# Optimization experiments

Hardware: AMD Instinct MI355X
Metric: run time of the kernel (lower is better)

Reference implementation:

```python
import jax, jax.numpy as jnp
import numpy as np

N_NODES = 50000
N_EDGES = 800000
D = 128


def _gcn_layer(x, src, dst, deg_inv_sqrt, W, b, n_nodes):
    # GCNConv: X' = D^{-1/2} (A + I) D^{-1/2} X W + b   (PyG default, self-loops added)
    h = x @ W  # [N, D]
    norm = deg_inv_sqrt[src] * deg_inv_sqrt[dst]  # [E+N]
    msgs = h[src] * norm[:, None]  # [E+N, D] gather + scale
    out = jax.ops.segment_sum(msgs, dst, num_segments=n_nodes)  # scatter-add
    return out + b


def setup_inputs() -> dict:
    key = jax.random.key(0)
    k1, k2, k3, k4 = jax.random.split(key, 4)
    x = jax.random.normal(k1, (N_NODES, D), dtype=jnp.float32)
    edge_index = jax.random.randint(k2, (2, N_EDGES), 0, N_NODES, dtype=jnp.int64)
    scale = 1.0 / np.sqrt(D)
    W1 = jax.random.normal(k3, (D, D), dtype=jnp.float32) * scale
    b1 = jnp.zeros((D,), dtype=jnp.float32)
    W2 = jax.random.normal(k4, (D, D), dtype=jnp.float32) * scale
    b2 = jnp.zeros((D,), dtype=jnp.float32)
    return {"x": x, "edge_index": edge_index, "W1": W1, "b1": b1, "W2": W2, "b2": b2}


def reference(x, edge_index, W1, b1, W2, b2):
    n_nodes = x.shape[0]
    # add self-loops once (same graph both layers)
    loop = jnp.arange(n_nodes, dtype=edge_index.dtype)
    src = jnp.concatenate([edge_index[0], loop])
    dst = jnp.concatenate([edge_index[1], loop])
    deg = jax.ops.segment_sum(jnp.ones_like(dst, dtype=x.dtype), dst, num_segments=n_nodes)
    deg_inv_sqrt = jnp.where(deg > 0, jax.lax.rsqrt(deg), 0.0)

    h = _gcn_layer(x, src, dst, deg_inv_sqrt, W1, b1, n_nodes)
    h = jax.nn.relu(h)
    h = _gcn_layer(h, src, dst, deg_inv_sqrt, W2, b2, n_nodes)
    h = jax.nn.relu(h)
    return h
```

## Files before the change

### kernel.cpp

```cpp
#include <hip/hip_runtime.h>

#define N_NODES 50000
#define N_EDGES 800000
#define D 128
#define NBKT 391
#define ACB 196
#define ACCHUNK 4096
#define BKTPAD 2432
#define GB 391
#define PB 3125
#define MAXDEG 64

typedef unsigned int uint32;
typedef unsigned short ushort;
typedef __attribute__((ext_vector_type(8))) short s8v;
typedef __attribute__((ext_vector_type(4))) float f4v;

__device__ __forceinline__ ushort f2bf(float f) {
    unsigned u = __float_as_uint(f);
    u += 0x7FFFu + ((u >> 16) & 1u);
    return (ushort)(u >> 16);
}
__device__ __forceinline__ float bf_lo(uint32 u) { return __uint_as_float(u << 16); }
__device__ __forceinline__ float bf_hi(uint32 u) { return __uint_as_float(u & 0xFFFF0000u); }

__global__ __launch_bounds__(256) void prep_kernel(int* __restrict__ bktCnt,
                                                   const float* __restrict__ W1,
                                                   const float* __restrict__ W2,
                                                   ushort* __restrict__ W1t,
                                                   ushort* __restrict__ W2t) {
    int t = threadIdx.x, blk = blockIdx.x;
    if (blk == 32) {
        for (int i = t; i < NBKT; i += 256) bktCnt[i] = 0;
        return;
    }
    const float* W = (blk >= 16) ? W2 : W1;
    ushort* Wt = (blk >= 16) ? W2t : W1t;
    int fid = (blk & 15) * 256 + t;
    int k = fid >> 5;
    int n0 = (fid & 31) * 4;
    float4 w = ((const float4*)W)[fid];
    Wt[(n0 + 0) * D + k] = f2bf(w.x);
    Wt[(n0 + 1) * D + k] = f2bf(w.y);
    Wt[(n0 + 2) * D + k] = f2bf(w.z);
    Wt[(n0 + 3) * D + k] = f2bf(w.w);
}

__global__ __launch_bounds__(256) void phaseAC_kernel(const int* __restrict__ src,
                                                      const int* __restrict__ dst,
                                                      int* __restrict__ bktCnt,
                                                      uint32* __restrict__ edgeTmp) {
    __shared__ int lc[NBKT];
    __shared__ int gb[NBKT];
    int t = threadIdx.x, blk = blockIdx.x;
    for (int i = t; i < NBKT; i += 256) lc[i] = 0;
    __syncthreads();
    uint32 ed[16];
    int e0 = blk * ACCHUNK;
    #pragma unroll
    for (int j = 0; j < 16; j++) {
        int e = e0 + t + j * 256;
        uint32 pk = 0xFFFFFFFFu;
        if (e < N_EDGES) {
            uint32 s = (uint32)src[e], d = (uint32)dst[e];
            pk = (s << 16) | d;
            atomicAdd(&lc[d >> 7], 1);
        }
        ed[j] = pk;
    }
    __syncthreads();
    for (int i = t; i < NBKT; i += 256) {
        int c = lc[i];
        gb[i] = (c > 0) ? atomicAdd(&bktCnt[i], c) : 0;
        lc[i] = 0;
    }
    __syncthreads();
    #pragma unroll
    for (int j = 0; j < 16; j++) {
        uint32 pk = ed[j];
        if (pk != 0xFFFFFFFFu) {
            int bkt = (int)(pk & 0xFFFFu) >> 7;
            int r = atomicAdd(&lc[bkt], 1);
            int idx = gb[bkt] + r;
            if (idx < BKTPAD) edgeTmp[bkt * BKTPAD + idx] = pk;
        }
    }
}

__global__ __launch_bounds__(256) void phaseDG_kernel(const uint32* __restrict__ edgeTmp,
                                                      const int* __restrict__ bktCnt,
                                                      int* __restrict__ deg,
                                                      ushort* __restrict__ e16,
                                                      const float* __restrict__ X,
                                                      const ushort* __restrict__ Wt,
                                                      ushort* __restrict__ Hb) {
    __shared__ int cnt[128];
    __shared__ int cur[128];
    __shared__ float disS[128];
    __shared__ ushort Cs[128 * 136];
    int t = threadIdx.x, b = blockIdx.x;
    int ce = bktCnt[b];
    int cntE = ce < BKTPAD ? ce : BKTPAD;
    int beg = b * BKTPAD, end = beg + cntE;
    if (t < 128) { cnt[t] = 0; cur[t] = 0; }
    __syncthreads();
    for (int p = beg + t; p < end; p += 256)
        atomicAdd(&cnt[edgeTmp[p] & 127], 1);
    __syncthreads();
    int node = b * 128 + t;
    if (t < 128) {
        int c = cnt[t];
        if (node < N_NODES) deg[node] = c;
        disS[t] = rsqrtf((float)c + 1.0f);
    }
    __syncthreads();
    for (int p = beg + t; p < end; p += 256) {
        uint32 u = edgeTmp[p];
        int loc = u & 127;
        int r = atomicAdd(&cur[loc], 1);
        if (r < MAXDEG) e16[((b * 128 + loc) << 6) + r] = (ushort)(u >> 16);
    }
    int wv = t >> 6, lane = t & 63;
    int q = lane >> 4, m = lane & 15;
    int rbase = b * 128 + wv * 32;
    f4v zero = {0.f, 0.f, 0.f, 0.f};
    f4v acc[2][8];
    #pragma unroll
    for (int mt = 0; mt < 2; mt++)
        #pragma unroll
        for (int n = 0; n < 8; n++) acc[mt][n] = zero;
    #pragma unroll
    for (int kt = 0; kt < 4; kt++) {
        int k0 = kt * 32 + q * 8;
        s8v a[2];
        #pragma unroll
        for (int mt = 0; mt < 2; mt++) {
            int row = rbase + mt * 16 + m;
            if (row >= N_NODES) row = N_NODES - 1;
            const float* xp = X + (size_t)row * D + k0;
            float4 u0 = *(const float4*)xp;
            float4 u1 = *(const float4*)(xp + 4);
            s8v av;
            av[0] = (short)f2bf(u0.x); av[1] = (short)f2bf(u0.y);
            av[2] = (short)f2bf(u0.z); av[3] = (short)f2bf(u0.w);
            av[4] = (short)f2bf(u1.x); av[5] = (short)f2bf(u1.y);
            av[6] = (short)f2bf(u1.z); av[7] = (short)f2bf(u1.w);
            a[mt] = av;
        }
        #pragma unroll
        for (int n = 0; n < 8; n++) {
            s8v bb = *(const s8v*)(Wt + (size_t)(n * 16 + m) * D + k0);
            acc[0][n] = __builtin_amdgcn_mfma_f32_16x16x32_bf16(a[0], bb, acc[0][n], 0, 0, 0);
            acc[1][n] = __builtin_amdgcn_mfma_f32_16x16x32_bf16(a[1], bb, acc[1][n], 0, 0, 0);
        }
    }
    __syncthreads();
    #pragma unroll
    for (int mt = 0; mt < 2; mt++)
        #pragma unroll
        for (int n = 0; n < 8; n++)
            #pragma unroll
            for (int r = 0; r < 4; r++) {
                int lr = wv * 32 + mt * 16 + q * 4 + r;
                Cs[lr * 136 + n * 16 + m] = f2bf(acc[mt][n][r] * disS[lr]);
            }
    __syncthreads();
    int gbase = b * 128;
    #pragma unroll
    for (int it = 0; it < 8; it++) {
        int cid = t + it * 256;
        int row = cid >> 4, off = (cid & 15) * 8;
        int grow = gbase + row;
        if (grow < N_NODES) {
            s8v v = *(const s8v*)(Cs + row * 136 + off);
            *(s8v*)(Hb + (size_t)grow * D + off) = v;
        }
    }
}

__global__ __launch_bounds__(256) void gemm_mfma(const ushort* __restrict__ Xb,
                                                 const ushort* __restrict__ Wt,
                                                 const int* __restrict__ deg,
                                                 ushort* __restrict__ Hb) {
    __shared__ ushort Cs[128 * 136];
    int t = threadIdx.x;
    int wv = t >> 6, lane = t & 63;
    int q = lane >> 4, m = lane & 15;
    int rbase = blockIdx.x * 128 + wv * 32;
    f4v zero = {0.f, 0.f, 0.f, 0.f};
    f4v acc[2][8];
    #pragma unroll
    for (int mt = 0; mt < 2; mt++)
        #pragma unroll
        for (int n = 0; n < 8; n++) acc[mt][n] = zero;

    #pragma unroll
    for (int kt = 0; kt < 4; kt++) {
        int k0 = kt * 32 + q * 8;
        s8v a[2];
        #pragma unroll
        for (int mt = 0; mt < 2; mt++) {
            int row = rbase + mt * 16 + m;
            if (row >= N_NODES) row = N_NODES - 1;
            a[mt] = *(const s8v*)(Xb + (size_t)row * D + k0);
        }
        #pragma unroll
        for (int n = 0; n < 8; n++) {
            s8v b = *(const s8v*)(Wt + (size_t)(n * 16 + m) * D + k0);
            acc[0][n] = __builtin_amdgcn_mfma_f32_16x16x32_bf16(a[0], b, acc[0][n], 0, 0, 0);
            acc[1][n] = __builtin_amdgcn_mfma_f32_16x16x32_bf16(a[1], b, acc[1][n], 0, 0, 0);
        }
    }
    float disv[2][4];
    #pragma unroll
    for (int mt = 0; mt < 2; mt++)
        #pragma unroll
        for (int r = 0; r < 4; r++) {
            int row = rbase + mt * 16 + q * 4 + r;
            if (row >= N_NODES) row = N_NODES - 1;
            disv[mt][r] = rsqrtf((float)deg[row] + 1.0f);
        }
    #pragma unroll
    for (int mt = 0; mt < 2; mt++)
        #pragma unroll
        for (int n = 0; n < 8; n++)
            #pragma unroll
            for (int r = 0; r < 4; r++) {
                int row = wv * 32 + mt * 16 + q * 4 + r;
                Cs[row * 136 + n * 16 + m] = f2bf(acc[mt][n][r] * disv[mt][r]);
            }
    __syncthreads();
    int gbase = blockIdx.x * 128;
    #pragma unroll
    for (int it = 0; it < 8; it++) {
        int cid = t + it * 256;
        int row = cid >> 4, off = (cid & 15) * 8;
        int grow = gbase + row;
        if (grow < N_NODES) {
            s8v v = *(const s8v*)(Cs + row * 136 + off);
            *(s8v*)(Hb + (size_t)grow * D + off) = v;
        }
    }
}

__device__ __forceinline__ void acc8(float* a, uint4 v) {
    a[0] += bf_lo(v.x); a[1] += bf_hi(v.x);
    a[2] += bf_lo(v.y); a[3] += bf_hi(v.y);
    a[4] += bf_lo(v.z); a[5] += bf_hi(v.z);
    a[6] += bf_lo(v.w); a[7] += bf_hi(v.w);
}

template<bool BF16OUT>
__global__ __launch_bounds__(256) void aggr_kernel(const uint4* __restrict__ Hb4,
                                                   const int* __restrict__ deg,
                                                   const ushort* __restrict__ e16,
                                                   const float* __restrict__ bias,
                                                   void* __restrict__ Hout) {
    int t = threadIdx.x;
    int li = t & 15;
    int n = blockIdx.x * 16 + (t >> 4);
    int dg = deg[n];
    float dn = rsqrtf((float)dg + 1.0f);
    float a[8];
    {
        uint4 sv = Hb4[(size_t)n * 16 + li];
        a[0] = bf_lo(sv.x); a[1] = bf_hi(sv.x);
        a[2] = bf_lo(sv.y); a[3] = bf_hi(sv.y);
        a[4] = bf_lo(sv.z); a[5] = bf_hi(sv.z);
        a[6] = bf_lo(sv.w); a[7] = bf_hi(sv.w);
    }
    int beg = n << 6;
    int end = beg + (dg < MAXDEG ? dg : MAXDEG);
    int p = beg;
    for (; p + 7 < end; p += 8) {
        int s[8];
        #pragma unroll
        for (int j = 0; j < 8; j++) s[j] = e16[p + j];
        uint4 v[8];
        #pragma unroll
        for (int j = 0; j < 8; j++) v[j] = Hb4[(size_t)s[j] * 16 + li];
        #pragma unroll
        for (int j = 0; j < 8; j++) acc8(a, v[j]);
    }
    for (; p + 3 < end; p += 4) {
        int s0 = e16[p + 0], s1 = e16[p + 1], s2 = e16[p + 2], s3 = e16[p + 3];
        uint4 v0 = Hb4[(size_t)s0 * 16 + li];
        uint4 v1 = Hb4[(size_t)s1 * 16 + li];
        uint4 v2 = Hb4[(size_t)s2 * 16 + li];
        uint4 v3 = Hb4[(size_t)s3 * 16 + li];
        acc8(a, v0); acc8(a, v1); acc8(a, v2); acc8(a, v3);
    }
    for (; p < end; p++) {
        uint4 v0 = Hb4[(size_t)e16[p] * 16 + li];
        acc8(a, v0);
    }
    const float4* b4 = (const float4*)bias;
    float4 bb0 = b4[li * 2], bb1 = b4[li * 2 + 1];
    float r0 = fmaxf(fmaf(dn, a[0], bb0.x), 0.f);
    float r1 = fmaxf(fmaf(dn, a[1], bb0.y), 0.f);
    float r2 = fmaxf(fmaf(dn, a[2], bb0.z), 0.f);
    float r3 = fmaxf(fmaf(dn, a[3], bb0.w), 0.f);
    float r4 = fmaxf(fmaf(dn, a[4], bb1.x), 0.f);
    float r5 = fmaxf(fmaf(dn, a[5], bb1.y), 0.f);
    float r6 = fmaxf(fmaf(dn, a[6], bb1.z), 0.f);
    float r7 = fmaxf(fmaf(dn, a[7], bb1.w), 0.f);
    if (BF16OUT) {
        uint4 o;
        o.x = (uint32)f2bf(r0) | ((uint32)f2bf(r1) << 16);
        o.y = (uint32)f2bf(r2) | ((uint32)f2bf(r3) << 16);
        o.z = (uint32)f2bf(r4) | ((uint32)f2bf(r5) << 16);
        o.w = (uint32)f2bf(r6) | ((uint32)f2bf(r7) << 16);
        ((uint4*)Hout)[(size_t)n * 16 + li] = o;
    } else {
        float4* H4 = (float4*)Hout;
        float4 o0; o0.x = r0; o0.y = r1; o0.z = r2; o0.w = r3;
        float4 o1; o1.x = r4; o1.y = r5; o1.z = r6; o1.w = r7;
        H4[(size_t)n * 32 + li * 2]     = o0;
        H4[(size_t)n * 32 + li * 2 + 1] = o1;
    }
}

extern "C" void kernel_launch(void* const* d_in, const int* in_sizes, int n_in,
                              void* d_out, int out_size, void* d_ws, size_t ws_size,
                              hipStream_t stream) {
    const float* x  = (const float*)d_in[0];
    const int*   ei = (const int*)d_in[1];
    const float* W1 = (const float*)d_in[2];
    const float* b1 = (const float*)d_in[3];
    const float* W2 = (const float*)d_in[4];
    const float* b2 = (const float*)d_in[5];
    float* out = (float*)d_out;

    char* ws = (char*)d_ws;
    size_t off = 0;
    auto alloc = [&](size_t bytes) -> void* {
        void* p = ws + off;
        off += (bytes + 255) & ~(size_t)255;
        return p;
    };
    int*    bktCnt  = (int*)alloc((size_t)NBKT * 4);
    uint32* edgeTmp = (uint32*)alloc((size_t)NBKT * BKTPAD * 4);
    int*    deg     = (int*)alloc((size_t)N_NODES * 4);
    ushort* e16     = (ushort*)alloc((size_t)N_NODES * MAXDEG * 2);
    ushort* Hb      = (ushort*)alloc((size_t)N_NODES * D * 2);
    ushort* HO1     = (ushort*)alloc((size_t)N_NODES * D * 2);
    ushort* W1t     = (ushort*)alloc((size_t)D * D * 2);
    ushort* W2t     = (ushort*)alloc((size_t)D * D * 2);
    ushort* Hb2     = Hb;

    const int* src = ei;
    const int* dst = ei + N_EDGES;

    prep_kernel<<<33, 256, 0, stream>>>(bktCnt, W1, W2, W1t, W2t);
    phaseAC_kernel<<<ACB, 256, 0, stream>>>(src, dst, bktCnt, edgeTmp);
    phaseDG_kernel<<<NBKT, 256, 0, stream>>>(edgeTmp, bktCnt, deg, e16, x, W1t, Hb);
    aggr_kernel<true><<<PB, 256, 0, stream>>>((const uint4*)Hb, deg, e16, b1, HO1);
    gemm_mfma<<<GB, 256, 0, stream>>>(HO1, W2t, deg, Hb2);
    aggr_kernel<false><<<PB, 256, 0, stream>>>((const uint4*)Hb2, deg, e16, b2, out);
}
```

Measured before the change: 200.7 us.

## Partition each node's neighbor list into four source-index ranges for gather locality

The CSR build now counts each node's edges in four chunks by source-node range and places them in range order, with per-chunk counts packed into a uint32 deg4 array. The aggregation kernel walks the neighbor list chunk by chunk, so concurrently running nodes tend to gather from the same quarter of the feature table at the same time, which should improve L2 locality. In exchange the 8-wide unrolled gather loop is dropped for a 4-wide loop per chunk. Packing counts into 8 bits assumes no chunk holds more than 255 edges for a node.

```diff
diff --git a/kernel.cpp b/kernel.cpp
--- a/kernel.cpp
+++ b/kernel.cpp
@@ -10,6 +10,7 @@
 #define GB 391
 #define PB 3125
 #define MAXDEG 64
+#define CHN 12500
 
 typedef unsigned int uint32;
 typedef unsigned short ushort;
@@ -90,35 +91,46 @@
 __global__ __launch_bounds__(256) void phaseDG_kernel(const uint32* __restrict__ edgeTmp,
                                                       const int* __restrict__ bktCnt,
                                                       int* __restrict__ deg,
+                                                      uint32* __restrict__ deg4,
                                                       ushort* __restrict__ e16,
                                                       const float* __restrict__ X,
                                                       const ushort* __restrict__ Wt,
                                                       ushort* __restrict__ Hb) {
-    __shared__ int cnt[128];
-    __shared__ int cur[128];
+    __shared__ int cnt4[128][4];
+    __shared__ int cur4[128][4];
     __shared__ float disS[128];
     __shared__ ushort Cs[128 * 136];
     int t = threadIdx.x, b = blockIdx.x;
     int ce = bktCnt[b];
     int cntE = ce < BKTPAD ? ce : BKTPAD;
     int beg = b * BKTPAD, end = beg + cntE;
-    if (t < 128) { cnt[t] = 0; cur[t] = 0; }
-    __syncthreads();
-    for (int p = beg + t; p < end; p += 256)
-        atomicAdd(&cnt[edgeTmp[p] & 127], 1);
+    if (t < 128) { cnt4[t][0] = 0; cnt4[t][1] = 0; cnt4[t][2] = 0; cnt4[t][3] = 0; }
+    __syncthreads();
+    for (int p = beg + t; p < end; p += 256) {
+        uint32 u = edgeTmp[p];
+        int ch = (int)(u >> 16) / CHN;
+        atomicAdd(&cnt4[u & 127][ch], 1);
+    }
     __syncthreads();
     int node = b * 128 + t;
     if (t < 128) {
-        int c = cnt[t];
-        if (node < N_NODES) deg[node] = c;
-        disS[t] = rsqrtf((float)c + 1.0f);
+        int c0 = cnt4[t][0], c1 = cnt4[t][1], c2 = cnt4[t][2], c3 = cnt4[t][3];
+        int tot = c0 + c1 + c2 + c3;
+        if (node < N_NODES) {
+            deg[node] = tot;
+            deg4[node] = (uint32)c0 | ((uint32)c1 << 8) | ((uint32)c2 << 16)
+                       | ((uint32)c3 << 24);
+        }
+        disS[t] = rsqrtf((float)tot + 1.0f);
+        cur4[t][0] = 0; cur4[t][1] = c0; cur4[t][2] = c0 + c1; cur4[t][3] = c0 + c1 + c2;
     }
     __syncthreads();
     for (int p = beg + t; p < end; p += 256) {
         uint32 u = edgeTmp[p];
         int loc = u & 127;
-        int r = atomicAdd(&cur[loc], 1);
-        if (r < MAXDEG) e16[((b * 128 + loc) << 6) + r] = (ushort)(u >> 16);
+        int s = (int)(u >> 16);
+        int r = atomicAdd(&cur4[loc][s / CHN], 1);
+        if (r < MAXDEG) e16[((b * 128 + loc) << 6) + r] = (ushort)s;
     }
     int wv = t >> 6, lane = t & 63;
     int q = lane >> 4, m = lane & 15;
@@ -252,15 +264,17 @@
 
 template<bool BF16OUT>
 __global__ __launch_bounds__(256) void aggr_kernel(const uint4* __restrict__ Hb4,
-                                                   const int* __restrict__ deg,
+                                                   const uint32* __restrict__ deg4v,
                                                    const ushort* __restrict__ e16,
                                                    const float* __restrict__ bias,
                                                    void* __restrict__ Hout) {
     int t = threadIdx.x;
     int li = t & 15;
     int n = blockIdx.x * 16 + (t >> 4);
-    int dg = deg[n];
-    float dn = rsqrtf((float)dg + 1.0f);
+    uint32 d4 = deg4v[n];
+    int cc0 = d4 & 255, cc1 = (d4 >> 8) & 255, cc2 = (d4 >> 16) & 255, cc3 = d4 >> 24;
+    int tot = cc0 + cc1 + cc2 + cc3;
+    float dn = rsqrtf((float)tot + 1.0f);
     float a[8];
     {
         uint4 sv = Hb4[(size_t)n * 16 + li];
@@ -270,29 +284,25 @@
         a[6] = bf_lo(sv.w); a[7] = bf_hi(sv.w);
     }
     int beg = n << 6;
-    int end = beg + (dg < MAXDEG ? dg : MAXDEG);
+    int cap = beg + MAXDEG;
+    int cc[4] = {cc0, cc1, cc2, cc3};
     int p = beg;
-    for (; p + 7 < end; p += 8) {
-        int s[8];
-        #pragma unroll
-        for (int j = 0; j < 8; j++) s[j] = e16[p + j];
-        uint4 v[8];
-        #pragma unroll
-        for (int j = 0; j < 8; j++) v[j] = Hb4[(size_t)s[j] * 16 + li];
-        #pragma unroll
-        for (int j = 0; j < 8; j++) acc8(a, v[j]);
-    }
-    for (; p + 3 < end; p += 4) {
-        int s0 = e16[p + 0], s1 = e16[p + 1], s2 = e16[p + 2], s3 = e16[p + 3];
-        uint4 v0 = Hb4[(size_t)s0 * 16 + li];
-        uint4 v1 = Hb4[(size_t)s1 * 16 + li];
-        uint4 v2 = Hb4[(size_t)s2 * 16 + li];
-        uint4 v3 = Hb4[(size_t)s3 * 16 + li];
-        acc8(a, v0); acc8(a, v1); acc8(a, v2); acc8(a, v3);
-    }
-    for (; p < end; p++) {
-        uint4 v0 = Hb4[(size_t)e16[p] * 16 + li];
-        acc8(a, v0);
+    #pragma unroll 1
+    for (int ch = 0; ch < 4; ch++) {
+        int e2 = p + cc[ch];
+        if (e2 > cap) e2 = cap;
+        for (; p + 3 < e2; p += 4) {
+            int s0 = e16[p + 0], s1 = e16[p + 1], s2 = e16[p + 2], s3 = e16[p + 3];
+            uint4 v0 = Hb4[(size_t)s0 * 16 + li];
+            uint4 v1 = Hb4[(size_t)s1 * 16 + li];
+            uint4 v2 = Hb4[(size_t)s2 * 16 + li];
+            uint4 v3 = Hb4[(size_t)s3 * 16 + li];
+            acc8(a, v0); acc8(a, v1); acc8(a, v2); acc8(a, v3);
+        }
+        for (; p < e2; p++) {
+            uint4 v0 = Hb4[(size_t)e16[p] * 16 + li];
+            acc8(a, v0);
+        }
     }
     const float4* b4 = (const float4*)bias;
     float4 bb0 = b4[li * 2], bb1 = b4[li * 2 + 1];
@@ -341,6 +351,7 @@
     int*    bktCnt  = (int*)alloc((size_t)NBKT * 4);
     uint32* edgeTmp = (uint32*)alloc((size_t)NBKT * BKTPAD * 4);
     int*    deg     = (int*)alloc((size_t)N_NODES * 4);
+    uint32* deg4    = (uint32*)alloc((size_t)N_NODES * 4);
     ushort* e16     = (ushort*)alloc((size_t)N_NODES * MAXDEG * 2);
     ushort* Hb      = (ushort*)alloc((size_t)N_NODES * D * 2);
     ushort* HO1     = (ushort*)alloc((size_t)N_NODES * D * 2);
@@ -353,8 +364,9 @@
 
     prep_kernel<<<33, 256, 0, stream>>>(bktCnt, W1, W2, W1t, W2t);
     phaseAC_kernel<<<ACB, 256, 0, stream>>>(src, dst, bktCnt, edgeTmp);
-    phaseDG_kernel<<<NBKT, 256, 0, stream>>>(edgeTmp, bktCnt, deg, e16, x, W1t, Hb);
-    aggr_kernel<true><<<PB, 256, 0, stream>>>((const uint4*)Hb, deg, e16, b1, HO1);
+    phaseDG_kernel<<<NBKT, 256, 0, stream>>>(edgeTmp, bktCnt, deg, deg4, e16,
+                                             x, W1t, Hb);
+    aggr_kernel<true><<<PB, 256, 0, stream>>>((const uint4*)Hb, deg4, e16, b1, HO1);
     gemm_mfma<<<GB, 256, 0, stream>>>(HO1, W2t, deg, Hb2);
-    aggr_kernel<false><<<PB, 256, 0, stream>>>((const uint4*)Hb2, deg, e16, b2, out);
-}
+    aggr_kernel<false><<<PB, 256, 0, stream>>>((const uint4*)Hb2, deg4, e16, b2, out);
+}
```

Measured after the change: 201.9 us. About the same (+0.6%).

## Fuse layer-1 aggregation with layer-2 GEMM in one kernel

Applied to the files above, without the earlier changes.

Merges the first aggregation kernel and the second-layer MFMA GEMM into a single kernel. Each 16-node block stages its aggregated bf16 rows in shared memory, multiplies them by W2 with MFMA, scales by the degree normalisation and writes Hb2. This removes one launch and the HBM round trip of the intermediate HO1 buffer. In exchange, each block re-reads the 32KB W2 (likely cache-resident) and runs only 16-row MFMA tiles.

```diff
diff --git a/kernel.cpp b/kernel.cpp
--- a/kernel.cpp
+++ b/kernel.cpp
@@ -7,7 +7,6 @@
 #define ACB 196
 #define ACCHUNK 4096
 #define BKTPAD 2432
-#define GB 391
 #define PB 3125
 #define MAXDEG 64
 
@@ -178,71 +177,6 @@
     }
 }
 
-__global__ __launch_bounds__(256) void gemm_mfma(const ushort* __restrict__ Xb,
-                                                 const ushort* __restrict__ Wt,
-                                                 const int* __restrict__ deg,
-                                                 ushort* __restrict__ Hb) {
-    __shared__ ushort Cs[128 * 136];
-    int t = threadIdx.x;
-    int wv = t >> 6, lane = t & 63;
-    int q = lane >> 4, m = lane & 15;
-    int rbase = blockIdx.x * 128 + wv * 32;
-    f4v zero = {0.f, 0.f, 0.f, 0.f};
-    f4v acc[2][8];
-    #pragma unroll
-    for (int mt = 0; mt < 2; mt++)
-        #pragma unroll
-        for (int n = 0; n < 8; n++) acc[mt][n] = zero;
-
-    #pragma unroll
-    for (int kt = 0; kt < 4; kt++) {
-        int k0 = kt * 32 + q * 8;
-        s8v a[2];
-        #pragma unroll
-        for (int mt = 0; mt < 2; mt++) {
-            int row = rbase + mt * 16 + m;
-            if (row >= N_NODES) row = N_NODES - 1;
-            a[mt] = *(const s8v*)(Xb + (size_t)row * D + k0);
-        }
-        #pragma unroll
-        for (int n = 0; n < 8; n++) {
-            s8v b = *(const s8v*)(Wt + (size_t)(n * 16 + m) * D + k0);
-            acc[0][n] = __builtin_amdgcn_mfma_f32_16x16x32_bf16(a[0], b, acc[0][n], 0, 0, 0);
-            acc[1][n] = __builtin_amdgcn_mfma_f32_16x16x32_bf16(a[1], b, acc[1][n], 0, 0, 0);
-        }
-    }
-    float disv[2][4];
-    #pragma unroll
-    for (int mt = 0; mt < 2; mt++)
-        #pragma unroll
-        for (int r = 0; r < 4; r++) {
-            int row = rbase + mt * 16 + q * 4 + r;
-            if (row >= N_NODES) row = N_NODES - 1;
-            disv[mt][r] = rsqrtf((float)deg[row] + 1.0f);
-        }
-    #pragma unroll
-    for (int mt = 0; mt < 2; mt++)
-        #pragma unroll
-        for (int n = 0; n < 8; n++)
-            #pragma unroll
-            for (int r = 0; r < 4; r++) {
-                int row = wv * 32 + mt * 16 + q * 4 + r;
-                Cs[row * 136 + n * 16 + m] = f2bf(acc[mt][n][r] * disv[mt][r]);
-            }
-    __syncthreads();
-    int gbase = blockIdx.x * 128;
-    #pragma unroll
-    for (int it = 0; it < 8; it++) {
-        int cid = t + it * 256;
-        int row = cid >> 4, off = (cid & 15) * 8;
-        int grow = gbase + row;
-        if (grow < N_NODES) {
-            s8v v = *(const s8v*)(Cs + row * 136 + off);
-            *(s8v*)(Hb + (size_t)grow * D + off) = v;
-        }
-    }
-}
-
 __device__ __forceinline__ void acc8(float* a, uint4 v) {
     a[0] += bf_lo(v.x); a[1] += bf_hi(v.x);
     a[2] += bf_lo(v.y); a[3] += bf_hi(v.y);
@@ -250,12 +184,100 @@
     a[6] += bf_lo(v.w); a[7] += bf_hi(v.w);
 }
 
-template<bool BF16OUT>
+__global__ __launch_bounds__(256) void aggrW2_kernel(const uint4* __restrict__ Hb4,
+                                                     const int* __restrict__ deg,
+                                                     const ushort* __restrict__ e16,
+                                                     const float* __restrict__ bias,
+                                                     const ushort* __restrict__ Wt,
+                                                     ushort* __restrict__ Hb2) {
+    __shared__ ushort Hs[16 * 136];
+    __shared__ ushort Cs[16 * 136];
+    __shared__ float disS[16];
+    int t = threadIdx.x;
+    int li = t & 15, g = t >> 4;
+    int n = blockIdx.x * 16 + g;
+    int dg = deg[n];
+    float dn = rsqrtf((float)dg + 1.0f);
+    if (li == 0) disS[g] = dn;
+    float a[8];
+    {
+        uint4 sv = Hb4[(size_t)n * 16 + li];
+        a[0] = bf_lo(sv.x); a[1] = bf_hi(sv.x);
+        a[2] = bf_lo(sv.y); a[3] = bf_hi(sv.y);
+        a[4] = bf_lo(sv.z); a[5] = bf_hi(sv.z);
+        a[6] = bf_lo(sv.w); a[7] = bf_hi(sv.w);
+    }
+    int beg = n << 6;
+    int end = beg + (dg < MAXDEG ? dg : MAXDEG);
+    int p = beg;
+    for (; p + 7 < end; p += 8) {
+        int s[8];
+        #pragma unroll
+        for (int j = 0; j < 8; j++) s[j] = e16[p + j];
+        uint4 v[8];
+        #pragma unroll
+        for (int j = 0; j < 8; j++) v[j] = Hb4[(size_t)s[j] * 16 + li];
+        #pragma unroll
+        for (int j = 0; j < 8; j++) acc8(a, v[j]);
+    }
+    for (; p + 3 < end; p += 4) {
+        int s0 = e16[p + 0], s1 = e16[p + 1], s2 = e16[p + 2], s3 = e16[p + 3];
+        uint4 v0 = Hb4[(size_t)s0 * 16 + li];
+        uint4 v1 = Hb4[(size_t)s1 * 16 + li];
+        uint4 v2 = Hb4[(size_t)s2 * 16 + li];
+        uint4 v3 = Hb4[(size_t)s3 * 16 + li];
+        acc8(a, v0); acc8(a, v1); acc8(a, v2); acc8(a, v3);
+    }
+    for (; p < end; p++) {
+        uint4 v0 = Hb4[(size_t)e16[p] * 16 + li];
+        acc8(a, v0);
+    }
+    const float4* b4 = (const float4*)bias;
+    float4 bb0 = b4[li * 2], bb1 = b4[li * 2 + 1];
+    s8v o;
+    o[0] = (short)f2bf(fmaxf(fmaf(dn, a[0], bb0.x), 0.f));
+    o[1] = (short)f2bf(fmaxf(fmaf(dn, a[1], bb0.y), 0.f));
+    o[2] = (short)f2bf(fmaxf(fmaf(dn, a[2], bb0.z), 0.f));
+    o[3] = (short)f2bf(fmaxf(fmaf(dn, a[3], bb0.w), 0.f));
+    o[4] = (short)f2bf(fmaxf(fmaf(dn, a[4], bb1.x), 0.f));
+    o[5] = (short)f2bf(fmaxf(fmaf(dn, a[5], bb1.y), 0.f));
+    o[6] = (short)f2bf(fmaxf(fmaf(dn, a[6], bb1.z), 0.f));
+    o[7] = (short)f2bf(fmaxf(fmaf(dn, a[7], bb1.w), 0.f));
+    *(s8v*)(Hs + g * 136 + li * 8) = o;
+    __syncthreads();
+    int wv = t >> 6, lane = t & 63;
+    int q = lane >> 4, m = lane & 15;
+    f4v zero = {0.f, 0.f, 0.f, 0.f};
+    f4v acc[2] = {zero, zero};
+    #pragma unroll
+    for (int kt = 0; kt < 4; kt++) {
+        int k0 = kt * 32 + q * 8;
+        s8v av = *(const s8v*)(Hs + m * 136 + k0);
+        #pragma unroll
+        for (int nt = 0; nt < 2; nt++) {
+            int col0 = (wv * 2 + nt) * 16;
+            s8v bv = *(const s8v*)(Wt + (size_t)(col0 + m) * D + k0);
+            acc[nt] = __builtin_amdgcn_mfma_f32_16x16x32_bf16(av, bv, acc[nt], 0, 0, 0);
+        }
+    }
+    #pragma unroll
+    for (int nt = 0; nt < 2; nt++)
+        #pragma unroll
+        for (int r = 0; r < 4; r++) {
+            int row = q * 4 + r;
+            Cs[row * 136 + (wv * 2 + nt) * 16 + m] = f2bf(acc[nt][r] * disS[row]);
+        }
+    __syncthreads();
+    int row = t >> 4, off = (t & 15) * 8;
+    *(s8v*)(Hb2 + (size_t)(blockIdx.x * 16 + row) * D + off) =
+        *(const s8v*)(Cs + row * 136 + off);
+}
+
 __global__ __launch_bounds__(256) void aggr_kernel(const uint4* __restrict__ Hb4,
                                                    const int* __restrict__ deg,
                                                    const ushort* __restrict__ e16,
                                                    const float* __restrict__ bias,
-                                                   void* __restrict__ Hout) {
+                                                   float* __restrict__ Hout) {
     int t = threadIdx.x;
     int li = t & 15;
     int n = blockIdx.x * 16 + (t >> 4);
@@ -296,28 +318,18 @@
     }
     const float4* b4 = (const float4*)bias;
     float4 bb0 = b4[li * 2], bb1 = b4[li * 2 + 1];
-    float r0 = fmaxf(fmaf(dn, a[0], bb0.x), 0.f);
-    float r1 = fmaxf(fmaf(dn, a[1], bb0.y), 0.f);
-    float r2 = fmaxf(fmaf(dn, a[2], bb0.z), 0.f);
-    float r3 = fmaxf(fmaf(dn, a[3], bb0.w), 0.f);
-    float r4 = fmaxf(fmaf(dn, a[4], bb1.x), 0.f);
-    float r5 = fmaxf(fmaf(dn, a[5], bb1.y), 0.f);
-    float r6 = fmaxf(fmaf(dn, a[6], bb1.z), 0.f);
-    float r7 = fmaxf(fmaf(dn, a[7], bb1.w), 0.f);
-    if (BF16OUT) {
-        uint4 o;
-        o.x = (uint32)f2bf(r0) | ((uint32)f2bf(r1) << 16);
-        o.y = (uint32)f2bf(r2) | ((uint32)f2bf(r3) << 16);
-        o.z = (uint32)f2bf(r4) | ((uint32)f2bf(r5) << 16);
-        o.w = (uint32)f2bf(r6) | ((uint32)f2bf(r7) << 16);
-        ((uint4*)Hout)[(size_t)n * 16 + li] = o;
-    } else {
-        float4* H4 = (float4*)Hout;
-        float4 o0; o0.x = r0; o0.y = r1; o0.z = r2; o0.w = r3;
-        float4 o1; o1.x = r4; o1.y = r5; o1.z = r6; o1.w = r7;
-        H4[(size_t)n * 32 + li * 2]     = o0;
-        H4[(size_t)n * 32 + li * 2 + 1] = o1;
-    }
+    float4 o0, o1;
+    o0.x = fmaxf(fmaf(dn, a[0], bb0.x), 0.f);
+    o0.y = fmaxf(fmaf(dn, a[1], bb0.y), 0.f);
+    o0.z = fmaxf(fmaf(dn, a[2], bb0.z), 0.f);
+    o0.w = fmaxf(fmaf(dn, a[3], bb0.w), 0.f);
+    o1.x = fmaxf(fmaf(dn, a[4], bb1.x), 0.f);
+    o1.y = fmaxf(fmaf(dn, a[5], bb1.y), 0.f);
+    o1.z = fmaxf(fmaf(dn, a[6], bb1.z), 0.f);
+    o1.w = fmaxf(fmaf(dn, a[7], bb1.w), 0.f);
+    float4* H4 = (float4*)Hout;
+    H4[(size_t)n * 32 + li * 2]     = o0;
+    H4[(size_t)n * 32 + li * 2 + 1] = o1;
 }
 
 extern "C" void kernel_launch(void* const* d_in, const int* in_sizes, int n_in,
@@ -343,10 +355,9 @@
     int*    deg     = (int*)alloc((size_t)N_NODES * 4);
     ushort* e16     = (ushort*)alloc((size_t)N_NODES * MAXDEG * 2);
     ushort* Hb      = (ushort*)alloc((size_t)N_NODES * D * 2);
-    ushort* HO1     = (ushort*)alloc((size_t)N_NODES * D * 2);
+    ushort* Hb2     = (ushort*)alloc((size_t)N_NODES * D * 2);
     ushort* W1t     = (ushort*)alloc((size_t)D * D * 2);
     ushort* W2t     = (ushort*)alloc((size_t)D * D * 2);
-    ushort* Hb2     = Hb;
 
     const int* src = ei;
     const int* dst = ei + N_EDGES;
@@ -354,7 +365,6 @@
     prep_kernel<<<33, 256, 0, stream>>>(bktCnt, W1, W2, W1t, W2t);
     phaseAC_kernel<<<ACB, 256, 0, stream>>>(src, dst, bktCnt, edgeTmp);
     phaseDG_kernel<<<NBKT, 256, 0, stream>>>(edgeTmp, bktCnt, deg, e16, x, W1t, Hb);
-    aggr_kernel<true><<<PB, 256, 0, stream>>>((const uint4*)Hb, deg, e16, b1, HO1);
-    gemm_mfma<<<GB, 256, 0, stream>>>(HO1, W2t, deg, Hb2);
-    aggr_kernel<false><<<PB, 256, 0, stream>>>((const uint4*)Hb2, deg, e16, b2, out);
-}
+    aggrW2_kernel<<<PB, 256, 0, stream>>>((const uint4*)Hb, deg, e16, b1, W2t, Hb2);
+    aggr_kernel<<<PB, 256, 0, stream>>>((const uint4*)Hb2, deg, e16, b2, out);
+}
```

New measurement: 189.0 us. 5.8% less time.
